# Kernel tuning notes

Measured on AMD Instinct MI355X. Metric: run time of the kernel, lower is better.

Reference implementation:

```python
import jax, jax.numpy as jnp
import numpy as np

B, T, D, H = 2, 2048, 1024, 16
HS = D // H  # head_size = 64
DFF = 4 * D


def setup_inputs() -> dict:
    key = jax.random.key(0)
    ks = jax.random.split(key, 12)
    s = 0.02
    return {
        "x": jax.random.normal(ks[0], (B, T, D), dtype=jnp.float32),
        "Wq": jax.random.normal(ks[1], (D, D), dtype=jnp.float32) * s,
        "Wk": jax.random.normal(ks[2], (D, D), dtype=jnp.float32) * s,
        "Wv": jax.random.normal(ks[3], (D, D), dtype=jnp.float32) * s,
        "Wo": jax.random.normal(ks[4], (D, D), dtype=jnp.float32) * s,
        "bo": jnp.zeros((D,), dtype=jnp.float32),
        "W1": jax.random.normal(ks[5], (D, DFF), dtype=jnp.float32) * s,
        "b1": jnp.zeros((DFF,), dtype=jnp.float32),
        "W2": jax.random.normal(ks[6], (DFF, D), dtype=jnp.float32) * s,
        "b2": jnp.zeros((D,), dtype=jnp.float32),
        "g1": jnp.ones((D,), dtype=jnp.float32),
        "be1": jnp.zeros((D,), dtype=jnp.float32),
        "g2": jnp.ones((D,), dtype=jnp.float32),
        "be2": jnp.zeros((D,), dtype=jnp.float32),
    }


def layer_norm(x, g, b, eps=1e-5):
    mu = jnp.mean(x, axis=-1, keepdims=True)
    var = jnp.var(x, axis=-1, keepdims=True)
    return (x - mu) * jax.lax.rsqrt(var + eps) * g + b


def attention(x, Wq, Wk, Wv, Wo, bo):
    # x: [B,T,D] -> q,k,v: [B,H,T,HS]
    def split_heads(y):
        return y.reshape(B, T, H, HS).transpose(0, 2, 1, 3)
    q = split_heads(x @ Wq)
    k = split_heads(x @ Wk)
    v = split_heads(x @ Wv)
    scores = jnp.einsum("bhqd,bhkd->bhqk", q, k) / jnp.sqrt(jnp.float32(HS))
    causal = jnp.tril(jnp.ones((T, T), dtype=bool))
    scores = jnp.where(causal, scores, -jnp.inf)
    probs = jax.nn.softmax(scores, axis=-1)
    out = jnp.einsum("bhqk,bhkd->bhqd", probs, v)
    out = out.transpose(0, 2, 1, 3).reshape(B, T, D)
    return out @ Wo + bo


def reference(x, Wq, Wk, Wv, Wo, bo, W1, b1, W2, b2, g1, be1, g2, be2):
    x = x + attention(layer_norm(x, g1, be1), Wq, Wk, Wv, Wo, bo)
    h = layer_norm(x, g2, be2)
    x = x + (jax.nn.relu(h @ W1 + b1) @ W2 + b2)
    return x
```

## Files before the change

### kernel.cpp

```cpp
#include <hip/hip_runtime.h>
#include <stdint.h>

#define Bc   2
#define Tc   2048
#define Dc   1024
#define Hc   16
#define HSc  64
#define DFFc 4096
#define Mc   (Bc * Tc)

using f32x4 = __attribute__((ext_vector_type(4))) float;
using s16x8 = __attribute__((ext_vector_type(8))) short;

__device__ __forceinline__ ushort f2bf(float f) {
  union { float f; uint32_t u; } v; v.f = f;
  uint32_t r = (v.u + 0x7FFFu + ((v.u >> 16) & 1u)) >> 16;
  return (ushort)r;
}
__device__ __forceinline__ float bf2f(ushort u) {
  union { uint32_t u; float f; } v; v.u = ((uint32_t)u) << 16;
  return v.f;
}
__device__ __forceinline__ uint32_t cvtpk(float a, float b) {
  uint32_t r;
  asm volatile("v_cvt_pk_bf16_f32 %0, %1, %2" : "=v"(r) : "v"(a), "v"(b));
  return r;
}
__device__ __forceinline__ float wredsum(float v) {
#pragma unroll
  for (int o = 32; o > 0; o >>= 1) v += __shfl_down(v, o);
  return v;
}

__device__ __forceinline__ void gload16(const ushort* g, ushort* l) {
  __builtin_amdgcn_global_load_lds(
      (const __attribute__((address_space(1))) void*)g,
      (__attribute__((address_space(3))) void*)l, 16, 0, 0);
}

template <int N> __device__ __forceinline__ void vwait() {
  if constexpr (N == 0) asm volatile("s_waitcnt vmcnt(0)" ::: "memory");
  else if constexpr (N == 6) asm volatile("s_waitcnt vmcnt(6)" ::: "memory");
  else asm volatile("s_waitcnt vmcnt(8)" ::: "memory");
}

__global__ __launch_bounds__(256) void tcast_all_kernel(
    const float* __restrict__ Wq, const float* __restrict__ Wk,
    const float* __restrict__ Wv, const float* __restrict__ Wo,
    const float* __restrict__ W1, const float* __restrict__ W2,
    ushort* __restrict__ wqkvt, ushort* __restrict__ wot,
    ushort* __restrict__ w1t, ushort* __restrict__ w2t) {
  __shared__ float t[32][33];
  const int id = blockIdx.x;
  const float* src; ushort* dst; int K, N, bx, by;
  if (id < 4096) {
    const int which = id >> 10, local = id & 1023;
    src = (which == 0) ? Wq : (which == 1) ? Wk : (which == 2) ? Wv : Wo;
    dst = (which == 3) ? wot : wqkvt + (size_t)which * 1024 * 1024;
    K = 1024; N = 1024; bx = local & 31; by = local >> 5;
  } else if (id < 8192) {
    const int local = id - 4096;
    src = W1; dst = w1t; K = 1024; N = 4096;
    bx = local & 127; by = local >> 7;
  } else {
    const int local = id - 8192;
    src = W2; dst = w2t; K = 4096; N = 1024;
    bx = local & 31; by = local >> 5;
  }
  const int tid = threadIdx.x;
  const int n0 = bx * 32, k0 = by * 32;
  const int r = tid >> 3, c4 = (tid & 7) * 4;
  const float4 v = *(const float4*)&src[(size_t)(k0 + r) * N + n0 + c4];
  t[r][c4] = v.x; t[r][c4 + 1] = v.y; t[r][c4 + 2] = v.z; t[r][c4 + 3] = v.w;
  __syncthreads();
  ushort4 o;
  o.x = f2bf(t[c4 + 0][r]); o.y = f2bf(t[c4 + 1][r]);
  o.z = f2bf(t[c4 + 2][r]); o.w = f2bf(t[c4 + 3][r]);
  *(ushort4*)&dst[(size_t)(n0 + r) * K + k0 + c4] = o;
}

__global__ __launch_bounds__(256) void ln_kernel(const float* __restrict__ x,
                                                 const float* __restrict__ g,
                                                 const float* __restrict__ b,
                                                 ushort* __restrict__ out) {
  const int row = blockIdx.x;
  const int tid = threadIdx.x;
  const int lane = tid & 63, wave = tid >> 6;
  const float4 v = ((const float4*)(x + (size_t)row * Dc))[tid];
  float s  = v.x + v.y + v.z + v.w;
  float s2 = v.x * v.x + v.y * v.y + v.z * v.z + v.w * v.w;
  __shared__ float rs[4], rs2[4];
  s = wredsum(s); s2 = wredsum(s2);
  if (lane == 0) { rs[wave] = s; rs2[wave] = s2; }
  __syncthreads();
  const float S  = rs[0] + rs[1] + rs[2] + rs[3];
  const float S2 = rs2[0] + rs2[1] + rs2[2] + rs2[3];
  const float mu = S * (1.f / (float)Dc);
  const float rstd = rsqrtf(S2 * (1.f / (float)Dc) - mu * mu + 1e-5f);
  const float4 gv = ((const float4*)g)[tid];
  const float4 bv = ((const float4*)b)[tid];
  ushort4 o;
  o.x = f2bf((v.x - mu) * rstd * gv.x + bv.x);
  o.y = f2bf((v.y - mu) * rstd * gv.y + bv.y);
  o.z = f2bf((v.z - mu) * rstd * gv.z + bv.z);
  o.w = f2bf((v.w - mu) * rstd * gv.w + bv.w);
  ((ushort4*)(out + (size_t)row * Dc))[tid] = o;
}

template <int BM, int NSPLIT, int OUT_BF16, int RELU, int BIAS, int RES, int QKVSPLIT>
__global__ __launch_bounds__(256) void gemm3_kernel(
    const ushort* __restrict__ A, const ushort* __restrict__ Bt,
    const float* __restrict__ bias, const float* __restrict__ res,
    void* __restrict__ C0, void* __restrict__ C1, void* __restrict__ C2,
    int M, int N, int K) {
  constexpr int MF = BM / 32;
  __shared__ __align__(16) ushort As[BM * 64];
  __shared__ __align__(16) ushort Bs[128 * 64];
  const int tid = threadIdx.x;
  const int lane = tid & 63, w = tid >> 6;
  const int wm = w >> 1, wn = w & 1;
  const int row0 = blockIdx.x * BM, col0 = blockIdx.y * 128;
  const int fr = lane & 15, fg = lane >> 4;
  const int kbeg = (NSPLIT > 1) ? blockIdx.z * (K / NSPLIT) : 0;
  const int kend = (NSPLIT > 1) ? kbeg + K / NSPLIT : K;

  f32x4 acc[MF][4] = {};

  for (int k0 = kbeg; k0 < kend; k0 += 64) {
#pragma unroll
    for (int i = 0; i < BM * 8 / 256; i++) {
      const int c = i * 256 + tid;
      const int r = c >> 3, j = c & 7;
      gload16(A + (size_t)(row0 + r) * K + k0 + ((j ^ (r & 7)) << 3),
              As + (i * 256 + w * 64) * 8);
    }
#pragma unroll
    for (int i = 0; i < 4; i++) {
      const int c = i * 256 + tid;
      const int r = c >> 3, j = c & 7;
      gload16(Bt + (size_t)(col0 + r) * K + k0 + ((j ^ (r & 7)) << 3),
              Bs + (i * 256 + w * 64) * 8);
    }
    __syncthreads();

#pragma unroll
    for (int kk = 0; kk < 2; kk++) {
      const int js = ((kk * 4 + fg) ^ (fr & 7)) << 3;
      s16x8 af[MF], bfr[4];
#pragma unroll
      for (int m = 0; m < MF; m++)
        af[m] = *(const s16x8*)&As[(wm * (BM / 2) + m * 16 + fr) * 64 + js];
#pragma unroll
      for (int n = 0; n < 4; n++)
        bfr[n] = *(const s16x8*)&Bs[(wn * 64 + n * 16 + fr) * 64 + js];
#pragma unroll
      for (int m = 0; m < MF; m++)
#pragma unroll
        for (int n = 0; n < 4; n++)
          acc[m][n] = __builtin_amdgcn_mfma_f32_16x16x32_bf16(af[m], bfr[n], acc[m][n], 0, 0, 0);
    }
    __syncthreads();
  }

  if (NSPLIT > 1) {
    float* P = (float*)C0 + (size_t)blockIdx.z * M * N;
#pragma unroll
    for (int m = 0; m < MF; m++)
#pragma unroll
      for (int n = 0; n < 4; n++)
#pragma unroll
        for (int i = 0; i < 4; i++) {
          const int r = row0 + wm * (BM / 2) + m * 16 + fg * 4 + i;
          const int c = col0 + n * 16 + wn * 64 + fr;
          P[(size_t)r * N + c] = acc[m][n][i];
        }
    return;
  }

  void* Cb = C0;
  int cbase = col0;
  if (QKVSPLIT) {
    const int which = col0 >> 10;
    Cb = (which == 0) ? C0 : (which == 1) ? C1 : C2;
    cbase = col0 & 1023;
  }
  const int NW = QKVSPLIT ? 1024 : N;
#pragma unroll
  for (int m = 0; m < MF; m++) {
#pragma unroll
    for (int n = 0; n < 4; n++) {
#pragma unroll
      for (int i = 0; i < 4; i++) {
        const int r = row0 + wm * (BM / 2) + m * 16 + fg * 4 + i;
        const int c = cbase + wn * 64 + n * 16 + fr;
        float v = acc[m][n][i];
        if (BIAS) v += bias[col0 - cbase + c];
        if (RELU) v = fmaxf(v, 0.f);
        if (RES)  v += res[(size_t)r * NW + c];
        if (OUT_BF16) ((ushort*)Cb)[(size_t)r * NW + c] = f2bf(v);
        else          ((float*)Cb)[(size_t)r * NW + c] = v;
      }
    }
  }
}

template <int BM, int NSPLIT, int OUT_BF16, int RELU, int BIAS, int RES, int QKVSPLIT>
__global__ __launch_bounds__(512, 2) void gemm8_kernel(
    const ushort* __restrict__ A, const ushort* __restrict__ Bt,
    const float* __restrict__ bias, const float* __restrict__ res,
    void* __restrict__ C0, void* __restrict__ C1, void* __restrict__ C2,
    int M, int N, int K) {
  constexpr int WR = BM / 2;
  constexpr int FI = WR / 16;
  constexpr int QF = FI / 2;
  constexpr int AIT = BM * 8 / 512;
  constexpr int LPT = AIT + 4;
  constexpr int BUFE = (BM + 256) * 64;
  __shared__ __align__(16) ushort lds[2 * BUFE];

  const int tid = threadIdx.x;
  const int lane = tid & 63, w = tid >> 6;
  const int wm = w >> 2, wn = w & 3;
  const int fr = lane & 15, fg = lane >> 4;
  const int row0 = blockIdx.x * BM, col0 = blockIdx.y * 256;
  const int kbeg = (NSPLIT > 1) ? blockIdx.z * (K / NSPLIT) : 0;
  const int nt = (K / NSPLIT) / 64;

  const int sr = tid >> 3;
  const int jswz = ((tid & 7) ^ (sr & 7)) << 3;

  f32x4 acc[FI][4] = {};

  auto STAGE = [&](int t, int buf) {
    const int k0 = kbeg + t * 64;
    ushort* base = lds + buf * BUFE;
    const ushort* ga = A + (size_t)(row0 + sr) * K + k0 + jswz;
#pragma unroll
    for (int i = 0; i < AIT; ++i)
      gload16(ga + (size_t)(i * 64) * K, base + (i * 512 + w * 64) * 8);
    const ushort* gb = Bt + (size_t)(col0 + sr) * K + k0 + jswz;
#pragma unroll
    for (int i = 0; i < 4; ++i)
      gload16(gb + (size_t)(i * 64) * K, base + BM * 64 + (i * 512 + w * 64) * 8);
  };

  auto COMPUTE = [&](int buf) {
    const ushort* ab = lds + buf * BUFE;
    const ushort* bb = ab + BM * 64;
#pragma unroll
    for (int q = 0; q < 2; ++q) {
      s16x8 af[QF][2];
#pragma unroll
      for (int fi = 0; fi < QF; ++fi) {
        const int arow = wm * WR + (q * QF + fi) * 16 + fr;
#pragma unroll
        for (int kk = 0; kk < 2; ++kk) {
          const int ck = (kk * 4 + fg) ^ (arow & 7);
          af[fi][kk] = *(const s16x8*)&ab[arow * 64 + ck * 8];
        }
      }
#pragma unroll
      for (int h = 0; h < 2; ++h) {
        s16x8 bf[2][2];
#pragma unroll
        for (int ni = 0; ni < 2; ++ni) {
          const int brow = wn * 64 + (h * 2 + ni) * 16 + fr;
#pragma unroll
          for (int kk = 0; kk < 2; ++kk) {
            const int ck = (kk * 4 + fg) ^ (brow & 7);
            bf[ni][kk] = *(const s16x8*)&bb[brow * 64 + ck * 8];
          }
        }
        __builtin_amdgcn_s_setprio(1);
#pragma unroll
        for (int fi = 0; fi < QF; ++fi)
#pragma unroll
          for (int ni = 0; ni < 2; ++ni)
#pragma unroll
            for (int kk = 0; kk < 2; ++kk)
              acc[q * QF + fi][h * 2 + ni] = __builtin_amdgcn_mfma_f32_16x16x32_bf16(
                  af[fi][kk], bf[ni][kk], acc[q * QF + fi][h * 2 + ni], 0, 0, 0);
        __builtin_amdgcn_s_setprio(0);
      }
    }
  };

  STAGE(0, 0);
  if (nt > 1) STAGE(1, 1);
  for (int t = 0; t < nt - 1; ++t) {
    const int cur = t & 1;
    vwait<LPT>();
    __builtin_amdgcn_sched_barrier(0);
    __builtin_amdgcn_s_barrier();
    __builtin_amdgcn_sched_barrier(0);
    COMPUTE(cur);
    __builtin_amdgcn_sched_barrier(0);
    __builtin_amdgcn_s_barrier();
    __builtin_amdgcn_sched_barrier(0);
    if (t + 2 < nt) STAGE(t + 2, cur);
  }
  vwait<0>();
  __builtin_amdgcn_sched_barrier(0);
  __builtin_amdgcn_s_barrier();
  __builtin_amdgcn_sched_barrier(0);
  COMPUTE((nt - 1) & 1);

  if constexpr (NSPLIT > 1) {
    float* P = (float*)C0 + (size_t)blockIdx.z * M * N;
#pragma unroll
    for (int mi = 0; mi < FI; ++mi)
#pragma unroll
      for (int ni = 0; ni < 4; ++ni)
#pragma unroll
        for (int i = 0; i < 4; ++i) {
          const int r = row0 + wm * WR + mi * 16 + fg * 4 + i;
          const int c = col0 + wn * 64 + ni * 16 + fr;
          P[(size_t)r * N + c] = acc[mi][ni][i];
        }
  } else {
    void* Cb = C0;
    int cbase = col0;
    if (QKVSPLIT) {
      const int which = col0 >> 10;
      Cb = (which == 0) ? C0 : (which == 1) ? C1 : C2;
      cbase = col0 & 1023;
    }
    const int NW = QKVSPLIT ? 1024 : N;
#pragma unroll
    for (int mi = 0; mi < FI; ++mi) {
#pragma unroll
      for (int ni = 0; ni < 4; ++ni) {
#pragma unroll
        for (int i = 0; i < 4; ++i) {
          const int r = row0 + wm * WR + mi * 16 + fg * 4 + i;
          const int c = cbase + wn * 64 + ni * 16 + fr;
          float v = acc[mi][ni][i];
          if (BIAS) v += bias[col0 - cbase + c];
          if (RELU) v = fmaxf(v, 0.f);
          if (RES)  v += res[(size_t)r * NW + c];
          if (OUT_BF16) ((ushort*)Cb)[(size_t)r * NW + c] = f2bf(v);
          else          ((float*)Cb)[(size_t)r * NW + c] = v;
        }
      }
    }
  }
}

__global__ __launch_bounds__(256) void sum2_kernel(const float* __restrict__ p0,
                                                   const float* __restrict__ p1,
                                                   const float* __restrict__ bias,
                                                   const float* __restrict__ res,
                                                   float* __restrict__ out) {
  const size_t i = ((size_t)blockIdx.x * 256 + threadIdx.x) * 4;
  const float4 a = *(const float4*)(p0 + i);
  const float4 b = *(const float4*)(p1 + i);
  const float4 r = *(const float4*)(res + i);
  const float4 bs = *(const float4*)(bias + (i & 1023));
  float4 o;
  o.x = a.x + b.x + bs.x + r.x;
  o.y = a.y + b.y + bs.y + r.y;
  o.z = a.z + b.z + bs.z + r.z;
  o.w = a.w + b.w + bs.w + r.w;
  *(float4*)(out + i) = o;
}

__global__ __launch_bounds__(512) void fattn3_kernel(const ushort* __restrict__ Q,
                                                     const ushort* __restrict__ K,
                                                     const ushort* __restrict__ V,
                                                     float* __restrict__ pacc,
                                                     float* __restrict__ pl) {
  __shared__ __align__(16) ushort Kl[2][64][72];
  __shared__ __align__(16) ushort Vt[2][64][72];
  __shared__ __align__(16) uint32_t Pu[8][512];

  const int tid = threadIdx.x;
  const int lane = tid & 63, w = tid >> 6;
  const int fr = lane & 15, fg = lane >> 4;

  const int bh   = blockIdx.x & 31;
  const int rest = blockIdx.x >> 5;
  const int qb   = 15 - (rest >> 1);
  const int z    = rest & 1;
  const int h = bh & 15, b = bh >> 4;
  const int q0 = qb * 128;
  const size_t hbase = (size_t)b * Tc * Dc + (size_t)h * HSc;

  s16x8 qf0, qf1;
  {
    const ushort* qp = Q + hbase + (size_t)(q0 + w * 16 + fr) * Dc + fg * 8;
    qf0 = *(const s16x8*)(qp);
    qf1 = *(const s16x8*)(qp + 32);
  }

  const int kkey = tid >> 3, kd8 = (tid & 7) * 8;
  const int vkey = tid & 63, vd8 = (tid >> 6) * 8;

  const int t0 = z * (qb + 1), t1 = (z + 1) * (qb + 1);
  uint4 kreg = *(const uint4*)(K + hbase + (size_t)(t0 * 64 + kkey) * Dc + kd8);
  uint4 vreg = *(const uint4*)(V + hbase + (size_t)(t0 * 64 + vkey) * Dc + vd8);

  f32x4 acc[4] = {};
  float ps = 0.f;
  const float Cs = 0.18033688f;

  for (int kt = t0; kt < t1; kt++) {
    const int cur = (kt - t0) & 1;
    *(uint4*)&Kl[cur][kkey][kd8] = kreg;
    {
      union { uint4 v; ushort u[8]; } t; t.v = vreg;
#pragma unroll
      for (int j = 0; j < 8; j++) Vt[cur][vd8 + j][vkey] = t.u[j];
    }
    if (kt + 1 < t1) {
      kreg = *(const uint4*)(K + hbase + (size_t)((kt + 1) * 64 + kkey) * Dc + kd8);
      vreg = *(const uint4*)(V + hbase + (size_t)((kt + 1) * 64 + vkey) * Dc + vd8);
    }
    __syncthreads();

    const bool skip = (kt * 64 > q0 + w * 16 + 15);
    if (!skip) {
      f32x4 s[4] = {};
      __builtin_amdgcn_s_setprio(1);
#pragma unroll
      for (int kf = 0; kf < 4; kf++) {
        const s16x8 k0 = *(const s16x8*)&Kl[cur][kf * 16 + fr][fg * 8];
        const s16x8 k1 = *(const s16x8*)&Kl[cur][kf * 16 + fr][32 + fg * 8];
        s[kf] = __builtin_amdgcn_mfma_f32_16x16x32_bf16(k0, qf0, s[kf], 0, 0, 0);
        s[kf] = __builtin_amdgcn_mfma_f32_16x16x32_bf16(k1, qf1, s[kf], 0, 0, 0);
      }
      __builtin_amdgcn_s_setprio(0);

      const bool diag = (kt * 64 + 63 > q0 + w * 16);
      const int qg = q0 + w * 16 + fr;
#pragma unroll
      for (int kf = 0; kf < 4; kf++) {
        float p[4];
#pragma unroll
        for (int i = 0; i < 4; i++) {
          p[i] = exp2f(s[kf][i] * Cs);
          if (diag) {
            const int kg = kt * 64 + kf * 16 + fg * 4 + i;
            if (kg > qg) p[i] = 0.f;
          }
          ps += p[i];
        }
        uint2 pk;
        pk.x = cvtpk(p[0], p[1]);
        pk.y = cvtpk(p[2], p[3]);
        *(uint2*)&Pu[w][(2 * kf + (fg >> 1)) * 64 + fr * 4 + (fg & 1) * 2] = pk;
      }

      const s16x8 pa0 = *(const s16x8*)&Pu[w][fg * 64 + fr * 4];
      const s16x8 pa1 = *(const s16x8*)&Pu[w][(4 + fg) * 64 + fr * 4];
      __builtin_amdgcn_s_setprio(1);
#pragma unroll
      for (int df = 0; df < 4; df++) {
        const s16x8 v0 = *(const s16x8*)&Vt[cur][df * 16 + fr][fg * 8];
        const s16x8 v1 = *(const s16x8*)&Vt[cur][df * 16 + fr][32 + fg * 8];
        acc[df] = __builtin_amdgcn_mfma_f32_16x16x32_bf16(pa0, v0, acc[df], 0, 0, 0);
        acc[df] = __builtin_amdgcn_mfma_f32_16x16x32_bf16(pa1, v1, acc[df], 0, 0, 0);
      }
      __builtin_amdgcn_s_setprio(0);
    }
  }

  ps += __shfl_xor(ps, 16);
  ps += __shfl_xor(ps, 32);
  if (lane < 16)
    pl[(size_t)z * (32 * 2048) + (size_t)bh * 2048 + q0 + w * 16 + lane] = ps;

  float* pa = pacc + (size_t)z * (32ull * 2048 * 64) + (size_t)bh * 2048 * 64;
#pragma unroll
  for (int i = 0; i < 4; i++) {
    const int qr = q0 + w * 16 + fg * 4 + i;
#pragma unroll
    for (int df = 0; df < 4; df++)
      pa[(size_t)qr * 64 + df * 16 + fr] = acc[df][i];
  }
}

__global__ __launch_bounds__(256) void amerge_kernel(const float* __restrict__ pacc,
                                                     const float* __restrict__ pl,
                                                     ushort* __restrict__ O) {
  const int g = blockIdx.x * 256 + threadIdx.x;
  const int d4 = g & 15;
  const int t  = (g >> 4) & 2047;
  const int bh = g >> 15;
  const int h = bh & 15, b = bh >> 4;
  const size_t base = ((size_t)bh * 2048 + t) * 64 + d4 * 4;
  const float4 a = *(const float4*)(pacc + base);
  const float4 c = *(const float4*)(pacc + 32ull * 2048 * 64 + base);
  const float inv = 1.f / (pl[(size_t)bh * 2048 + t] + pl[32 * 2048 + (size_t)bh * 2048 + t]);
  ushort4 o;
  o.x = f2bf((a.x + c.x) * inv);
  o.y = f2bf((a.y + c.y) * inv);
  o.z = f2bf((a.z + c.z) * inv);
  o.w = f2bf((a.w + c.w) * inv);
  *(ushort4*)&O[((size_t)(b * 2048 + t)) * 1024 + h * 64 + d4 * 4] = o;
}

extern "C" void kernel_launch(void* const* d_in, const int* in_sizes, int n_in,
                              void* d_out, int out_size, void* d_ws, size_t ws_size,
                              hipStream_t stream) {
  const float* x   = (const float*)d_in[0];
  const float* Wq  = (const float*)d_in[1];
  const float* Wk  = (const float*)d_in[2];
  const float* Wv  = (const float*)d_in[3];
  const float* Wo  = (const float*)d_in[4];
  const float* bo  = (const float*)d_in[5];
  const float* W1  = (const float*)d_in[6];
  const float* b1  = (const float*)d_in[7];
  const float* W2  = (const float*)d_in[8];
  const float* b2  = (const float*)d_in[9];
  const float* g1  = (const float*)d_in[10];
  const float* be1 = (const float*)d_in[11];
  const float* g2  = (const float*)d_in[12];
  const float* be2 = (const float*)d_in[13];

  char* ws = (char*)d_ws;
  const size_t MB = 1ull << 20;
  ushort* ln1   = (ushort*)(ws + 0 * MB);
  ushort* qb    = (ushort*)(ws + 8 * MB);
  ushort* kb    = (ushort*)(ws + 16 * MB);
  ushort* vb    = (ushort*)(ws + 24 * MB);
  ushort* wqkvt = (ushort*)(ws + 32 * MB);
  ushort* wot   = (ushort*)(ws + 38 * MB);
  ushort* w1t   = (ushort*)(ws + 40 * MB);
  ushort* w2t   = (ushort*)(ws + 48 * MB);
  float*  x1    = (float*)(ws + 56 * MB);
  ushort* hb    = (ushort*)(ws + 72 * MB);
  float*  pacc  = (float*)(ws + 56 * MB);
  float*  plv   = (float*)(ws + 88 * MB);
  float*  fpart = (float*)(ws + 0 * MB);

  tcast_all_kernel<<<12288, 256, 0, stream>>>(Wq, Wk, Wv, Wo, W1, W2,
                                              wqkvt, wot, w1t, w2t);

  ln_kernel<<<Mc, 256, 0, stream>>>(x, g1, be1, ln1);

  gemm8_kernel<256, 1, 1, 0, 0, 0, 1><<<dim3(16, 12), 512, 0, stream>>>(
      ln1, wqkvt, nullptr, nullptr, qb, kb, vb, Mc, 3072, Dc);

  fattn3_kernel<<<1024, 512, 0, stream>>>(qb, kb, vb, pacc, plv);
  amerge_kernel<<<4096, 256, 0, stream>>>(pacc, plv, ln1);

  gemm3_kernel<64, 1, 0, 0, 1, 1, 0><<<dim3(64, 8), 256, 0, stream>>>(
      ln1, wot, bo, x, x1, nullptr, nullptr, Mc, Dc, Dc);

  ln_kernel<<<Mc, 256, 0, stream>>>(x1, g2, be2, qb);

  gemm8_kernel<256, 1, 1, 1, 1, 0, 0><<<dim3(16, 16), 512, 0, stream>>>(
      qb, w1t, b1, nullptr, hb, nullptr, nullptr, Mc, DFFc, Dc);

  gemm8_kernel<128, 2, 0, 0, 0, 0, 0><<<dim3(32, 4, 2), 512, 0, stream>>>(
      hb, w2t, nullptr, nullptr, fpart, nullptr, nullptr, Mc, Dc, DFFc);
  sum2_kernel<<<4096, 256, 0, stream>>>(fpart, fpart + (size_t)Mc * Dc, b2, x1,
                                        (float*)d_out);
}
```

Baseline: 216.6 us.

## Restructure GEMM mainloop into 4-slot K=32 pipeline with interleaved prefetch

Replaces the double-buffered K=64 GEMM mainloop with a four-slot ring of K=32 stages, three tiles in flight, and a new XOR swizzle. Prefetch for stage s+3 is issued between A-fragment loads and the MFMA burst, split across the two M-phases when BM allows. The aim is deeper latency hiding of global-to-LDS loads at the same LDS footprint. In exchange it adds two barriers per phase and halves the MFMA work per barrier, which may raise synchronisation overhead.

```diff
diff --git a/kernel.cpp b/kernel.cpp
--- a/kernel.cpp
+++ b/kernel.cpp
@@ -40,8 +40,10 @@
 
 template <int N> __device__ __forceinline__ void vwait() {
   if constexpr (N == 0) asm volatile("s_waitcnt vmcnt(0)" ::: "memory");
+  else if constexpr (N == 3) asm volatile("s_waitcnt vmcnt(3)" ::: "memory");
+  else if constexpr (N == 4) asm volatile("s_waitcnt vmcnt(4)" ::: "memory");
   else if constexpr (N == 6) asm volatile("s_waitcnt vmcnt(6)" ::: "memory");
-  else asm volatile("s_waitcnt vmcnt(8)" ::: "memory");
+  else if constexpr (N == 8) asm volatile("s_waitcnt vmcnt(8)" ::: "memory");
 }
 
 __global__ __launch_bounds__(256) void tcast_all_kernel(
@@ -212,11 +214,11 @@
     int M, int N, int K) {
   constexpr int WR = BM / 2;
   constexpr int FI = WR / 16;
-  constexpr int QF = FI / 2;
-  constexpr int AIT = BM * 8 / 512;
-  constexpr int LPT = AIT + 4;
-  constexpr int BUFE = (BM + 256) * 64;
-  __shared__ __align__(16) ushort lds[2 * BUFE];
+  constexpr int NPH = FI / 4;
+  constexpr int APASS = BM / 128;
+  constexpr int LPS = APASS + 2;
+  constexpr int SLOT = (BM + 256) * 32;
+  __shared__ __align__(16) ushort lds[4 * SLOT];
 
   const int tid = threadIdx.x;
   const int lane = tid & 63, w = tid >> 6;
@@ -224,86 +226,91 @@
   const int fr = lane & 15, fg = lane >> 4;
   const int row0 = blockIdx.x * BM, col0 = blockIdx.y * 256;
   const int kbeg = (NSPLIT > 1) ? blockIdx.z * (K / NSPLIT) : 0;
-  const int nt = (K / NSPLIT) / 64;
-
-  const int sr = tid >> 3;
-  const int jswz = ((tid & 7) ^ (sr & 7)) << 3;
+  const int nt = (K / NSPLIT) / 32;
+
+  const int scc = tid & 3;
+  const int sr0 = tid >> 2;
 
   f32x4 acc[FI][4] = {};
 
-  auto STAGE = [&](int t, int buf) {
-    const int k0 = kbeg + t * 64;
-    ushort* base = lds + buf * BUFE;
-    const ushort* ga = A + (size_t)(row0 + sr) * K + k0 + jswz;
-#pragma unroll
-    for (int i = 0; i < AIT; ++i)
-      gload16(ga + (size_t)(i * 64) * K, base + (i * 512 + w * 64) * 8);
-    const ushort* gb = Bt + (size_t)(col0 + sr) * K + k0 + jswz;
-#pragma unroll
-    for (int i = 0; i < 4; ++i)
-      gload16(gb + (size_t)(i * 64) * K, base + BM * 64 + (i * 512 + w * 64) * 8);
+  auto STAGE_A = [&](int t) {
+    const int k0 = kbeg + t * 32;
+    ushort* base = lds + (size_t)(t & 3) * SLOT;
+#pragma unroll
+    for (int i = 0; i < APASS; ++i) {
+      const int r = i * 128 + sr0;
+      const int j = scc ^ ((r >> 1) & 3);
+      gload16(A + (size_t)(row0 + r) * K + k0 + j * 8,
+              base + (i * 512 + w * 64) * 8);
+    }
   };
-
-  auto COMPUTE = [&](int buf) {
-    const ushort* ab = lds + buf * BUFE;
-    const ushort* bb = ab + BM * 64;
-#pragma unroll
-    for (int q = 0; q < 2; ++q) {
-      s16x8 af[QF][2];
-#pragma unroll
-      for (int fi = 0; fi < QF; ++fi) {
-        const int arow = wm * WR + (q * QF + fi) * 16 + fr;
-#pragma unroll
-        for (int kk = 0; kk < 2; ++kk) {
-          const int ck = (kk * 4 + fg) ^ (arow & 7);
-          af[fi][kk] = *(const s16x8*)&ab[arow * 64 + ck * 8];
-        }
-      }
-#pragma unroll
-      for (int h = 0; h < 2; ++h) {
-        s16x8 bf[2][2];
-#pragma unroll
-        for (int ni = 0; ni < 2; ++ni) {
-          const int brow = wn * 64 + (h * 2 + ni) * 16 + fr;
-#pragma unroll
-          for (int kk = 0; kk < 2; ++kk) {
-            const int ck = (kk * 4 + fg) ^ (brow & 7);
-            bf[ni][kk] = *(const s16x8*)&bb[brow * 64 + ck * 8];
-          }
-        }
-        __builtin_amdgcn_s_setprio(1);
-#pragma unroll
-        for (int fi = 0; fi < QF; ++fi)
-#pragma unroll
-          for (int ni = 0; ni < 2; ++ni)
-#pragma unroll
-            for (int kk = 0; kk < 2; ++kk)
-              acc[q * QF + fi][h * 2 + ni] = __builtin_amdgcn_mfma_f32_16x16x32_bf16(
-                  af[fi][kk], bf[ni][kk], acc[q * QF + fi][h * 2 + ni], 0, 0, 0);
-        __builtin_amdgcn_s_setprio(0);
-      }
+  auto STAGE_B = [&](int t) {
+    const int k0 = kbeg + t * 32;
+    ushort* base = lds + (size_t)(t & 3) * SLOT + BM * 32;
+#pragma unroll
+    for (int i = 0; i < 2; ++i) {
+      const int r = i * 128 + sr0;
+      const int j = scc ^ ((r >> 1) & 3);
+      gload16(Bt + (size_t)(col0 + r) * K + k0 + j * 8,
+              base + (i * 512 + w * 64) * 8);
     }
   };
 
-  STAGE(0, 0);
-  if (nt > 1) STAGE(1, 1);
-  for (int t = 0; t < nt - 1; ++t) {
-    const int cur = t & 1;
-    vwait<LPT>();
-    __builtin_amdgcn_sched_barrier(0);
-    __builtin_amdgcn_s_barrier();
-    __builtin_amdgcn_sched_barrier(0);
-    COMPUTE(cur);
-    __builtin_amdgcn_sched_barrier(0);
-    __builtin_amdgcn_s_barrier();
-    __builtin_amdgcn_sched_barrier(0);
-    if (t + 2 < nt) STAGE(t + 2, cur);
-  }
-  vwait<0>();
+  STAGE_A(0); STAGE_B(0);
+  STAGE_A(1); STAGE_B(1);
+  STAGE_A(2); STAGE_B(2);
+  vwait<2 * LPS>();
   __builtin_amdgcn_sched_barrier(0);
   __builtin_amdgcn_s_barrier();
   __builtin_amdgcn_sched_barrier(0);
-  COMPUTE((nt - 1) & 1);
+
+  for (int s = 0; s < nt; ++s) {
+    const ushort* sb = lds + (size_t)(s & 3) * SLOT;
+    s16x8 bf[4];
+#pragma unroll
+    for (int ni = 0; ni < 4; ++ni) {
+      const int rb = wn * 64 + ni * 16 + fr;
+      const int ch = fg ^ ((rb >> 1) & 3);
+      bf[ni] = *(const s16x8*)&sb[BM * 32 + rb * 32 + ch * 8];
+    }
+#pragma unroll
+    for (int mh = 0; mh < NPH; ++mh) {
+      s16x8 af[4];
+#pragma unroll
+      for (int mi = 0; mi < 4; ++mi) {
+        const int ra = wm * WR + mh * 64 + mi * 16 + fr;
+        const int ch = fg ^ ((ra >> 1) & 3);
+        af[mi] = *(const s16x8*)&sb[ra * 32 + ch * 8];
+      }
+      if (s + 3 < nt) {
+        if constexpr (NPH == 2) {
+          if (mh == 0) STAGE_A(s + 3); else STAGE_B(s + 3);
+        } else {
+          STAGE_A(s + 3); STAGE_B(s + 3);
+        }
+      }
+      __builtin_amdgcn_sched_barrier(0);
+      __builtin_amdgcn_s_barrier();
+      __builtin_amdgcn_sched_barrier(0);
+      __builtin_amdgcn_s_setprio(1);
+#pragma unroll
+      for (int mi = 0; mi < 4; ++mi)
+#pragma unroll
+        for (int ni = 0; ni < 4; ++ni)
+          acc[mh * 4 + mi][ni] = __builtin_amdgcn_mfma_f32_16x16x32_bf16(
+              af[mi], bf[ni], acc[mh * 4 + mi][ni], 0, 0, 0);
+      __builtin_amdgcn_s_setprio(0);
+      __builtin_amdgcn_sched_barrier(0);
+      if (mh == NPH - 1) {
+        const int rem = nt - 2 - s;
+        if (rem >= 2) vwait<2 * LPS>();
+        else if (rem == 1) vwait<LPS>();
+        else if (rem == 0) vwait<0>();
+      }
+      __builtin_amdgcn_s_barrier();
+      __builtin_amdgcn_sched_barrier(0);
+    }
+  }
 
   if constexpr (NSPLIT > 1) {
     float* P = (float*)C0 + (size_t)blockIdx.z * M * N;
```

New measurement: 214.4 us. Within noise of the previous version (-1.0%).
